# Performance work log

Hardware: AMD Instinct MI355X
Metric: run time of the kernel (lower is better)

Reference implementation:

```python
import jax, jax.numpy as jnp
import numpy as np

BETA = 0.25

def setup_inputs() -> dict:
    key = jax.random.key(0)
    k1, k2 = jax.random.split(key)
    x = jax.random.normal(k1, (16, 4096, 256), dtype=jnp.float32)
    emb = jax.random.normal(k2, (8, 1024, 256), dtype=jnp.float32)
    return {"x": x, "emb": emb}

def _quantize(r_flat, e):
    # r_flat: [N, D], e: [K, D]
    # squared-distance matrix: ||r||^2 + ||e||^2 - 2 r.e^T  -> [N, K]
    d = (jnp.sum(r_flat * r_flat, axis=1, keepdims=True)
         + jnp.sum(e * e, axis=1)
         - 2.0 * r_flat @ e.T)
    idx = jnp.argmin(d, axis=1)          # [N]
    z_q = jnp.take(e, idx, axis=0)       # [N, D] gather
    return z_q, idx

def reference(x, emb):
    # x: [B, T, D]; emb: [Q, K, D]
    B, T, D = x.shape
    Q = emb.shape[0]
    sg = jax.lax.stop_gradient
    residual = x
    quantized_out = jnp.zeros_like(x)
    total_loss = jnp.zeros((), dtype=x.dtype)
    indices = []
    for i in range(Q):  # sequential residual dependency (small fixed Q)
        r_flat = residual.reshape(-1, D)
        zq_flat, idx = _quantize(r_flat, emb[i])
        z_q = zq_flat.reshape(residual.shape)
        loss = (BETA * jnp.mean((sg(z_q) - residual) ** 2)
                + jnp.mean((z_q - sg(residual)) ** 2))
        z_q = residual + sg(z_q - residual)  # straight-through
        residual = residual - z_q
        quantized_out = quantized_out + z_q
        total_loss = total_loss + loss
        indices.append(idx.reshape(B, T))
    return quantized_out, total_loss, jnp.stack(indices, axis=-1)
```

## Files before the change

kernel.cpp:

```cpp
#include <hip/hip_runtime.h>


#define NROWS 65536
#define DDIM  256
#define KC    1024
#define QST   8
#define BR    64
#define MCAP  24

typedef __attribute__((ext_vector_type(8))) short short8;
typedef __attribute__((ext_vector_type(4))) float f32x4;
typedef unsigned int u32;
typedef unsigned short u16;

__device__ __forceinline__ u16 f2bf(float f) {
  u32 b = __float_as_uint(f);
  return (u16)((b + 0x7FFFu + ((b >> 16) & 1u)) >> 16);
}
__device__ __forceinline__ float bf2f(u16 h) {
  return __uint_as_float(((u32)h) << 16);
}
__device__ __forceinline__ u32 runit(int row, int u) {
  return (u32)(row * 1024 + ((u ^ (row & 7)) << 4));
}
__device__ __forceinline__ void gld16(const void* g, void* lds) {
  __builtin_amdgcn_global_load_lds((const __attribute__((address_space(1))) u32*)g,
                                   (__attribute__((address_space(3))) u32*)lds, 16, 0, 0);
}

__global__ void e2_kernel(const float* __restrict__ emb, float* __restrict__ e2) {
  const int row  = blockIdx.x * 4 + (threadIdx.x >> 6);
  const int lane = threadIdx.x & 63;
  const float4 v = ((const float4*)(emb + (size_t)row * DDIM))[lane];
  float s = v.x * v.x + v.y * v.y + v.z * v.z + v.w * v.w;
  #pragma unroll
  for (int m = 32; m >= 1; m >>= 1) s += __shfl_xor(s, m);
  if (lane == 0) e2[row] = s;
}

__global__ void pack_kernel(const float* __restrict__ emb, u16* __restrict__ packE) {
  const int t = blockIdx.x * 256 + threadIdx.x;
  const int l   = t & 63;
  const int ci  = (t >> 6) & 3;
  const int ekt = (t >> 8) & 7;
  const int ct  = (t >> 11) & 15;
  const int qi  = t >> 15;
  const int code = ct * 64 + ci * 16 + (l & 15);
  const int d0   = ekt * 32 + (l >> 4) * 8;
  const float* src = emb + ((size_t)qi * KC + code) * DDIM + d0;
  short8 v;
  #pragma unroll
  for (int j = 0; j < 8; ++j) v[j] = (short)f2bf(src[j]);
  *(short8*)(packE + (size_t)t * 8) = v;
}

__global__ __launch_bounds__(512, 2)
void rvq_kernel(const float* __restrict__ x, const float* __restrict__ emb,
                const char* __restrict__ packEb, const float* __restrict__ e2g,
                float* __restrict__ out, float* __restrict__ outIdx,
                float* __restrict__ lossPart)
{
  __shared__ __align__(16) u16  Rl[BR * 512];
  __shared__ __align__(16) char Bbuf[8][2][4096];
  __shared__ float e2L[KC];
  __shared__ float sredV[8][BR];
  __shared__ int   sredI[8][BR];
  __shared__ float d0L[BR];
  __shared__ int   cntL[BR];
  __shared__ int   candL[BR][MCAP];
  __shared__ int   sidx[BR];
  __shared__ float rnormL[BR];
  __shared__ float redbuf[8];

  const int tid = threadIdx.x;
  const int w = tid >> 6, l = tid & 63;
  const int g = l >> 4, rb16 = l & 15;
  const int row = tid >> 3, sub = tid & 7;
  const size_t rowBase = (size_t)blockIdx.x * BR;
  char* RlB = (char*)Rl;
  float lossAcc = 0.f;
  float r[32];

  {
    const float* xp = x + (rowBase + row) * DDIM + 32 * sub;
    float rn = 0.f;
    #pragma unroll
    for (int uu = 0; uu < 4; ++uu) {
      f32x4 va = *(const f32x4*)(xp + 8 * uu);
      f32x4 vb = *(const f32x4*)(xp + 8 * uu + 4);
      r[8*uu+0]=va.x; r[8*uu+1]=va.y; r[8*uu+2]=va.z; r[8*uu+3]=va.w;
      r[8*uu+4]=vb.x; r[8*uu+5]=vb.y; r[8*uu+6]=vb.z; r[8*uu+7]=vb.w;
      short8 hv, lv;
      #pragma unroll
      for (int j = 0; j < 8; ++j) {
        float v = r[8*uu+j];
        u16 h = f2bf(v); float hf = bf2f(h);
        hv[j] = (short)h; lv[j] = (short)f2bf(v - hf);
        rn += v * v;
      }
      *(short8*)(RlB + runit(row, 4*sub + uu))      = hv;
      *(short8*)(RlB + runit(row, 32 + 4*sub + uu)) = lv;
    }
    rn += __shfl_xor(rn, 1); rn += __shfl_xor(rn, 2); rn += __shfl_xor(rn, 4);
    if (sub == 0) rnormL[row] = rn;
  }
  __syncthreads();

  for (int qi = 0; qi < QST; ++qi) {
    e2L[tid]       = e2g[qi * KC + tid];
    e2L[tid + 512] = e2g[qi * KC + 512 + tid];
    __syncthreads();

    f32x4 acc[2][4][4];
    #pragma unroll
    for (int a = 0; a < 2; ++a)
      #pragma unroll
      for (int b = 0; b < 4; ++b)
        #pragma unroll
        for (int c2 = 0; c2 < 4; ++c2)
          acc[a][b][c2] = (f32x4){0.f, 0.f, 0.f, 0.f};

    const size_t stageBase = ((size_t)qi * 16 + 2 * w) * 8 * 4096;
    #define CHUNK_SRC(c) (packEb + stageBase + (size_t)(c) * 4096 + (size_t)l * 16)
    #define ISSUE(c) do { \
      const char* _g = CHUNK_SRC(c); \
      char* _d = &Bbuf[w][(c) & 1][0]; \
      gld16(_g,        _d);        gld16(_g + 1024, _d + 1024); \
      gld16(_g + 2048, _d + 2048); gld16(_g + 3072, _d + 3072); \
    } while (0)

    ISSUE(0);
    #pragma unroll
    for (int c = 0; c < 16; ++c) {
      if (c < 15) { ISSUE(c + 1); asm volatile("s_waitcnt vmcnt(4)" ::: "memory"); }
      else        {               asm volatile("s_waitcnt vmcnt(0)" ::: "memory"); }
      const char* bufc = &Bbuf[w][c & 1][0];
      const int ekt = c & 7, ctl = c >> 3;
      short8 Af[4];
      #pragma unroll
      for (int ci = 0; ci < 4; ++ci)
        Af[ci] = *(const short8*)(bufc + ci * 1024 + l * 16);
      #pragma unroll
      for (int ri = 0; ri < 4; ++ri) {
        short8 B = *(const short8*)(RlB + runit(16 * ri + rb16, ekt * 4 + g));
        #pragma unroll
        for (int ci = 0; ci < 4; ++ci)
          acc[ctl][ci][ri] = __builtin_amdgcn_mfma_f32_16x16x32_bf16(Af[ci], B, acc[ctl][ci][ri], 0, 0, 0);
      }
      #pragma unroll
      for (int ri = 0; ri < 4; ++ri) {
        short8 B = *(const short8*)(RlB + runit(16 * ri + rb16, 32 + ekt * 4 + g));
        #pragma unroll
        for (int ci = 0; ci < 4; ++ci)
          acc[ctl][ci][ri] = __builtin_amdgcn_mfma_f32_16x16x32_bf16(Af[ci], B, acc[ctl][ci][ri], 0, 0, 0);
      }
    }

    float bestV[4]; int bestI[4];
    #pragma unroll
    for (int ri = 0; ri < 4; ++ri) { bestV[ri] = 3.4e38f; bestI[ri] = 0; }
    #pragma unroll
    for (int ctl = 0; ctl < 2; ++ctl) {
      const int cb = (2 * w + ctl) * 64;
      #pragma unroll
      for (int ci = 0; ci < 4; ++ci) {
        f32x4 e4 = *(const f32x4*)&e2L[cb + 16 * ci + 4 * g];
        #pragma unroll
        for (int j = 0; j < 4; ++j) {
          const int code = cb + 16 * ci + 4 * g + j;
          #pragma unroll
          for (int ri = 0; ri < 4; ++ri) {
            float d = e4[j] - 2.f * acc[ctl][ci][ri][j];
            if (d < bestV[ri]) { bestV[ri] = d; bestI[ri] = code; }
          }
        }
      }
    }
    #pragma unroll
    for (int m = 16; m <= 32; m <<= 1) {
      #pragma unroll
      for (int ri = 0; ri < 4; ++ri) {
        float ov = __shfl_xor(bestV[ri], m);
        int   oi = __shfl_xor(bestI[ri], m);
        if (ov < bestV[ri] || (ov == bestV[ri] && oi < bestI[ri])) { bestV[ri] = ov; bestI[ri] = oi; }
      }
    }
    if (l < 16) {
      #pragma unroll
      for (int ri = 0; ri < 4; ++ri) { sredV[w][16*ri + l] = bestV[ri]; sredI[w][16*ri + l] = bestI[ri]; }
    }
    __syncthreads();

    if (tid < BR) {
      float dv = sredV[0][tid]; int di = sredI[0][tid];
      #pragma unroll
      for (int wv = 1; wv < 8; ++wv) {
        float v = sredV[wv][tid]; int ii = sredI[wv][tid];
        if (v < dv || (v == dv && ii < di)) { dv = v; di = ii; }
      }
      d0L[tid] = dv; sidx[tid] = di; cntL[tid] = 0;
    }
    __syncthreads();

    {
      float thr[4];
      #pragma unroll
      for (int ri = 0; ri < 4; ++ri) {
        const int rw = 16 * ri + rb16;
        thr[ri] = d0L[rw] + 0.36f * sqrtf(rnormL[rw]) + 0.05f;
      }
      #pragma unroll
      for (int ctl = 0; ctl < 2; ++ctl) {
        const int cb = (2 * w + ctl) * 64;
        #pragma unroll
        for (int ci = 0; ci < 4; ++ci) {
          f32x4 e4 = *(const f32x4*)&e2L[cb + 16 * ci + 4 * g];
          #pragma unroll
          for (int ri = 0; ri < 4; ++ri) {
            #pragma unroll
            for (int j = 0; j < 4; ++j) {
              float d = e4[j] - 2.f * acc[ctl][ci][ri][j];
              if (d <= thr[ri]) {
                const int rw = 16 * ri + rb16;
                int p = atomicAdd(&cntL[rw], 1);
                if (p < MCAP) candL[rw][p] = cb + 16 * ci + 4 * g + j;
              }
            }
          }
        }
      }
    }
    __syncthreads();

    {
      int cnt = cntL[row];
      if (cnt > 1) {
        if (cnt > MCAP) cnt = MCAP;
        float bd = 3.4e38f; int bi = 0x7fffffff;
        for (int k2 = 0; k2 < cnt; ++k2) {
          const int c = candL[row][k2];
          const float* ep = emb + ((size_t)qi * KC + c) * DDIM + 32 * sub;
          float dot = 0.f;
          #pragma unroll
          for (int f = 0; f < 8; ++f) {
            f32x4 ev = *(const f32x4*)(ep + 4 * f);
            dot += r[4*f+0]*ev.x + r[4*f+1]*ev.y + r[4*f+2]*ev.z + r[4*f+3]*ev.w;
          }
          dot += __shfl_xor(dot, 1); dot += __shfl_xor(dot, 2); dot += __shfl_xor(dot, 4);
          float d = e2L[c] - 2.f * dot;
          if (d < bd || (d == bd && c < bi)) { bd = d; bi = c; }
        }
        if (sub == 0) sidx[row] = bi;
      }
    }
    __syncthreads();

    {
      const int c = sidx[row];
      const float* ep = emb + ((size_t)qi * KC + c) * DDIM + 32 * sub;
      float ls = 0.f;
      #pragma unroll
      for (int f = 0; f < 8; ++f) {
        f32x4 ev = *(const f32x4*)(ep + 4 * f);
        r[4*f+0] -= ev.x; ls += r[4*f+0]*r[4*f+0];
        r[4*f+1] -= ev.y; ls += r[4*f+1]*r[4*f+1];
        r[4*f+2] -= ev.z; ls += r[4*f+2]*r[4*f+2];
        r[4*f+3] -= ev.w; ls += r[4*f+3]*r[4*f+3];
      }
      #pragma unroll
      for (int uu = 0; uu < 4; ++uu) {
        short8 hv, lv;
        #pragma unroll
        for (int j = 0; j < 8; ++j) {
          float v = r[8*uu+j];
          u16 h = f2bf(v); float hf = bf2f(h);
          hv[j] = (short)h; lv[j] = (short)f2bf(v - hf);
        }
        *(short8*)(RlB + runit(row, 4*sub + uu))      = hv;
        *(short8*)(RlB + runit(row, 32 + 4*sub + uu)) = lv;
      }
      float rn = ls;
      rn += __shfl_xor(rn, 1); rn += __shfl_xor(rn, 2); rn += __shfl_xor(rn, 4);
      if (sub == 0) rnormL[row] = rn;
      lossAcc += ls;
      if (tid < BR) outIdx[(rowBase + tid) * QST + qi] = (float)sidx[tid];
    }
    __syncthreads();
  }

  {
    const float* xp = x + (rowBase + row) * DDIM + 32 * sub;
    float* op = out + (rowBase + row) * DDIM + 32 * sub;
    #pragma unroll
    for (int f = 0; f < 8; ++f) {
      f32x4 xv = *(const f32x4*)(xp + 4 * f);
      f32x4 o;
      o.x = xv.x - r[4*f+0]; o.y = xv.y - r[4*f+1];
      o.z = xv.z - r[4*f+2]; o.w = xv.w - r[4*f+3];
      *(f32x4*)(op + 4 * f) = o;
    }
  }

  {
    float s = lossAcc;
    #pragma unroll
    for (int m = 32; m >= 1; m >>= 1) s += __shfl_xor(s, m);
    if (l == 0) redbuf[w] = s;
    __syncthreads();
    if (tid == 0) {
      float t2 = 0.f;
      #pragma unroll
      for (int wv = 0; wv < 8; ++wv) t2 += redbuf[wv];
      lossPart[blockIdx.x] = t2;
    }
  }
}

__global__ void loss_final(const float* __restrict__ part, float* __restrict__ outLoss) {
  __shared__ float buf[256];
  const int t = threadIdx.x;
  float s = 0.f;
  #pragma unroll
  for (int k = 0; k < 4; ++k) s += part[t + 256 * k];
  buf[t] = s;
  __syncthreads();
  for (int st = 128; st >= 1; st >>= 1) {
    if (t < st) buf[t] += buf[t + st];
    __syncthreads();
  }
  if (t == 0) *outLoss = buf[0] * (1.25f / 16777216.f);
}

extern "C" void kernel_launch(void* const* d_in, const int* in_sizes, int n_in,
                              void* d_out, int out_size, void* d_ws, size_t ws_size,
                              hipStream_t stream) {
  (void)in_sizes; (void)n_in; (void)out_size; (void)ws_size;
  const float* x   = (const float*)d_in[0];
  const float* emb = (const float*)d_in[1];
  float* out     = (float*)d_out;
  float* outLoss = out + (size_t)NROWS * DDIM;
  float* outIdx  = outLoss + 1;
  char*  packE   = (char*)d_ws;
  float* e2      = (float*)(packE + (size_t)QST*16*8*4*4096);
  float* part    = e2 + QST * KC;

  pack_kernel<<<dim3(1024), dim3(256), 0, stream>>>(emb, (u16*)packE);
  e2_kernel<<<dim3(QST * KC / 4), dim3(256), 0, stream>>>(emb, e2);
  rvq_kernel<<<dim3(NROWS / BR), dim3(512), 0, stream>>>(x, emb, packE, e2, out, outIdx, part);
  loss_final<<<dim3(1), dim3(256), 0, stream>>>(part, outLoss);
}
```

Before: 984.2 us.

## Drop bf16 hi/lo split residual and use 16 waves per block

The residual is now kept in LDS as a single bf16 copy instead of a hi+lo split pair, which halves the MFMA work in the distance GEMM. The block grows to 1024 threads (16 waves), each wave owning 64 codes with a 4-deep async LDS prefetch ring, and each row is handled by 16 threads. The lower-precision distances lean more on the existing candidate threshold refinement, and a new fallback scans all 1024 codes in fp32 when candidates overflow MCAP. That fallback keeps results exact but can be expensive if the threshold admits too many candidates.

```diff
diff --git a/kernel.cpp b/kernel.cpp
--- a/kernel.cpp
+++ b/kernel.cpp
@@ -17,11 +17,8 @@
   u32 b = __float_as_uint(f);
   return (u16)((b + 0x7FFFu + ((b >> 16) & 1u)) >> 16);
 }
-__device__ __forceinline__ float bf2f(u16 h) {
-  return __uint_as_float(((u32)h) << 16);
-}
 __device__ __forceinline__ u32 runit(int row, int u) {
-  return (u32)(row * 1024 + ((u ^ (row & 7)) << 4));
+  return (u32)(row * 512 + ((u ^ (row & 7)) << 4));
 }
 __device__ __forceinline__ void gld16(const void* g, void* lds) {
   __builtin_amdgcn_global_load_lds((const __attribute__((address_space(1))) u32*)g,
@@ -39,140 +36,112 @@
 }
 
 __global__ void pack_kernel(const float* __restrict__ emb, u16* __restrict__ packE) {
-  const int t = blockIdx.x * 256 + threadIdx.x;
-  const int l   = t & 63;
-  const int ci  = (t >> 6) & 3;
-  const int ekt = (t >> 8) & 7;
-  const int ct  = (t >> 11) & 15;
-  const int qi  = t >> 15;
-  const int code = ct * 64 + ci * 16 + (l & 15);
-  const int d0   = ekt * 32 + (l >> 4) * 8;
-  const float* src = emb + ((size_t)qi * KC + code) * DDIM + d0;
+  const int t  = blockIdx.x * 256 + threadIdx.x;
+  const int l  = t & 63;
+  const int c  = (t >> 6) & 31;
+  const int w  = (t >> 11) & 15;
+  const int qi = t >> 15;
+  const int code = 64 * w + 16 * (c & 3) + (l & 15);
+  const int k    = 32 * (c >> 2) + 8 * (l >> 4);
+  const float* src = emb + ((size_t)qi * KC + code) * DDIM + k;
   short8 v;
   #pragma unroll
   for (int j = 0; j < 8; ++j) v[j] = (short)f2bf(src[j]);
   *(short8*)(packE + (size_t)t * 8) = v;
 }
 
-__global__ __launch_bounds__(512, 2)
+__global__ __launch_bounds__(1024)
 void rvq_kernel(const float* __restrict__ x, const float* __restrict__ emb,
                 const char* __restrict__ packEb, const float* __restrict__ e2g,
                 float* __restrict__ out, float* __restrict__ outIdx,
                 float* __restrict__ lossPart)
 {
-  __shared__ __align__(16) u16  Rl[BR * 512];
-  __shared__ __align__(16) char Bbuf[8][2][4096];
+  __shared__ __align__(16) u16  Rh[BR * 256];
+  __shared__ __align__(16) char Bbuf[16][4][1024];
   __shared__ float e2L[KC];
-  __shared__ float sredV[8][BR];
-  __shared__ int   sredI[8][BR];
+  __shared__ float sredV[16][BR];
+  __shared__ int   sredI[16][BR];
   __shared__ float d0L[BR];
   __shared__ int   cntL[BR];
   __shared__ int   candL[BR][MCAP];
   __shared__ int   sidx[BR];
   __shared__ float rnormL[BR];
-  __shared__ float redbuf[8];
+  __shared__ float red[16];
 
   const int tid = threadIdx.x;
   const int w = tid >> 6, l = tid & 63;
-  const int g = l >> 4, rb16 = l & 15;
-  const int row = tid >> 3, sub = tid & 7;
+  const int row = tid >> 4, sub = tid & 15;
   const size_t rowBase = (size_t)blockIdx.x * BR;
-  char* RlB = (char*)Rl;
+  char* RhB = (char*)Rh;
   float lossAcc = 0.f;
-  float r[32];
+  float r[16];
 
   {
-    const float* xp = x + (rowBase + row) * DDIM + 32 * sub;
+    const float* xp = x + (rowBase + row) * DDIM + 16 * sub;
     float rn = 0.f;
     #pragma unroll
-    for (int uu = 0; uu < 4; ++uu) {
-      f32x4 va = *(const f32x4*)(xp + 8 * uu);
-      f32x4 vb = *(const f32x4*)(xp + 8 * uu + 4);
-      r[8*uu+0]=va.x; r[8*uu+1]=va.y; r[8*uu+2]=va.z; r[8*uu+3]=va.w;
-      r[8*uu+4]=vb.x; r[8*uu+5]=vb.y; r[8*uu+6]=vb.z; r[8*uu+7]=vb.w;
-      short8 hv, lv;
-      #pragma unroll
-      for (int j = 0; j < 8; ++j) {
-        float v = r[8*uu+j];
-        u16 h = f2bf(v); float hf = bf2f(h);
-        hv[j] = (short)h; lv[j] = (short)f2bf(v - hf);
-        rn += v * v;
-      }
-      *(short8*)(RlB + runit(row, 4*sub + uu))      = hv;
-      *(short8*)(RlB + runit(row, 32 + 4*sub + uu)) = lv;
-    }
-    rn += __shfl_xor(rn, 1); rn += __shfl_xor(rn, 2); rn += __shfl_xor(rn, 4);
+    for (int f = 0; f < 4; ++f) {
+      f32x4 v = *(const f32x4*)(xp + 4 * f);
+      r[4*f+0] = v.x; r[4*f+1] = v.y; r[4*f+2] = v.z; r[4*f+3] = v.w;
+      rn += v.x*v.x + v.y*v.y + v.z*v.z + v.w*v.w;
+    }
+    short8 h0, h1;
+    #pragma unroll
+    for (int j = 0; j < 8; ++j) { h0[j] = (short)f2bf(r[j]); h1[j] = (short)f2bf(r[8+j]); }
+    *(short8*)(RhB + runit(row, 2*sub))     = h0;
+    *(short8*)(RhB + runit(row, 2*sub + 1)) = h1;
+    rn += __shfl_xor(rn, 1); rn += __shfl_xor(rn, 2);
+    rn += __shfl_xor(rn, 4); rn += __shfl_xor(rn, 8);
     if (sub == 0) rnormL[row] = rn;
   }
   __syncthreads();
 
   for (int qi = 0; qi < QST; ++qi) {
-    e2L[tid]       = e2g[qi * KC + tid];
-    e2L[tid + 512] = e2g[qi * KC + 512 + tid];
-    __syncthreads();
-
-    f32x4 acc[2][4][4];
-    #pragma unroll
-    for (int a = 0; a < 2; ++a)
-      #pragma unroll
-      for (int b = 0; b < 4; ++b)
+    e2L[tid] = e2g[qi * KC + tid];
+
+    f32x4 acc[4][4];
+    #pragma unroll
+    for (int a = 0; a < 4; ++a)
+      #pragma unroll
+      for (int b = 0; b < 4; ++b) acc[a][b] = (f32x4){0.f, 0.f, 0.f, 0.f};
+
+    const char* src = packEb + ((size_t)(qi * 16 + w) * 32) * 1024 + (size_t)l * 16;
+    #define ISSUE(c) gld16(src + (size_t)(c) * 1024, &Bbuf[w][(c) & 3][0])
+    ISSUE(0); ISSUE(1); ISSUE(2);
+    for (int ekt = 0; ekt < 8; ++ekt) {
+      short8 Bf[4];
+      #pragma unroll
+      for (int ri = 0; ri < 4; ++ri)
+        Bf[ri] = *(const short8*)(RhB + runit(16 * ri + (l & 15), ekt * 4 + (l >> 4)));
+      #pragma unroll
+      for (int ci = 0; ci < 4; ++ci) {
+        const int c = ekt * 4 + ci;
+        if (c < 29)      { ISSUE(c + 3); asm volatile("s_waitcnt vmcnt(3)" ::: "memory"); }
+        else if (c == 29) asm volatile("s_waitcnt vmcnt(2)" ::: "memory");
+        else if (c == 30) asm volatile("s_waitcnt vmcnt(1)" ::: "memory");
+        else              asm volatile("s_waitcnt vmcnt(0)" ::: "memory");
+        const short8 Af = *(const short8*)(&Bbuf[w][c & 3][l * 16]);
         #pragma unroll
-        for (int c2 = 0; c2 < 4; ++c2)
-          acc[a][b][c2] = (f32x4){0.f, 0.f, 0.f, 0.f};
-
-    const size_t stageBase = ((size_t)qi * 16 + 2 * w) * 8 * 4096;
-    #define CHUNK_SRC(c) (packEb + stageBase + (size_t)(c) * 4096 + (size_t)l * 16)
-    #define ISSUE(c) do { \
-      const char* _g = CHUNK_SRC(c); \
-      char* _d = &Bbuf[w][(c) & 1][0]; \
-      gld16(_g,        _d);        gld16(_g + 1024, _d + 1024); \
-      gld16(_g + 2048, _d + 2048); gld16(_g + 3072, _d + 3072); \
-    } while (0)
-
-    ISSUE(0);
-    #pragma unroll
-    for (int c = 0; c < 16; ++c) {
-      if (c < 15) { ISSUE(c + 1); asm volatile("s_waitcnt vmcnt(4)" ::: "memory"); }
-      else        {               asm volatile("s_waitcnt vmcnt(0)" ::: "memory"); }
-      const char* bufc = &Bbuf[w][c & 1][0];
-      const int ekt = c & 7, ctl = c >> 3;
-      short8 Af[4];
-      #pragma unroll
-      for (int ci = 0; ci < 4; ++ci)
-        Af[ci] = *(const short8*)(bufc + ci * 1024 + l * 16);
-      #pragma unroll
-      for (int ri = 0; ri < 4; ++ri) {
-        short8 B = *(const short8*)(RlB + runit(16 * ri + rb16, ekt * 4 + g));
+        for (int ri = 0; ri < 4; ++ri)
+          acc[ci][ri] = __builtin_amdgcn_mfma_f32_16x16x32_bf16(Af, Bf[ri], acc[ci][ri], 0, 0, 0);
+      }
+    }
+    #undef ISSUE
+    __syncthreads();
+
+    float bestV[4]; int bestI[4];
+    #pragma unroll
+    for (int ri = 0; ri < 4; ++ri) { bestV[ri] = 3.4e38f; bestI[ri] = 0; }
+    #pragma unroll
+    for (int ci = 0; ci < 4; ++ci) {
+      const int cb = 64 * w + 16 * ci + 4 * (l >> 4);
+      f32x4 e4 = *(const f32x4*)&e2L[cb];
+      #pragma unroll
+      for (int jj = 0; jj < 4; ++jj) {
         #pragma unroll
-        for (int ci = 0; ci < 4; ++ci)
-          acc[ctl][ci][ri] = __builtin_amdgcn_mfma_f32_16x16x32_bf16(Af[ci], B, acc[ctl][ci][ri], 0, 0, 0);
-      }
-      #pragma unroll
-      for (int ri = 0; ri < 4; ++ri) {
-        short8 B = *(const short8*)(RlB + runit(16 * ri + rb16, 32 + ekt * 4 + g));
-        #pragma unroll
-        for (int ci = 0; ci < 4; ++ci)
-          acc[ctl][ci][ri] = __builtin_amdgcn_mfma_f32_16x16x32_bf16(Af[ci], B, acc[ctl][ci][ri], 0, 0, 0);
-      }
-    }
-
-    float bestV[4]; int bestI[4];
-    #pragma unroll
-    for (int ri = 0; ri < 4; ++ri) { bestV[ri] = 3.4e38f; bestI[ri] = 0; }
-    #pragma unroll
-    for (int ctl = 0; ctl < 2; ++ctl) {
-      const int cb = (2 * w + ctl) * 64;
-      #pragma unroll
-      for (int ci = 0; ci < 4; ++ci) {
-        f32x4 e4 = *(const f32x4*)&e2L[cb + 16 * ci + 4 * g];
-        #pragma unroll
-        for (int j = 0; j < 4; ++j) {
-          const int code = cb + 16 * ci + 4 * g + j;
-          #pragma unroll
-          for (int ri = 0; ri < 4; ++ri) {
-            float d = e4[j] - 2.f * acc[ctl][ci][ri][j];
-            if (d < bestV[ri]) { bestV[ri] = d; bestI[ri] = code; }
-          }
+        for (int ri = 0; ri < 4; ++ri) {
+          float d = e4[jj] - 2.f * acc[ci][ri][jj];
+          if (d < bestV[ri]) { bestV[ri] = d; bestI[ri] = cb + jj; }
         }
       }
     }
@@ -194,7 +163,7 @@
     if (tid < BR) {
       float dv = sredV[0][tid]; int di = sredI[0][tid];
       #pragma unroll
-      for (int wv = 1; wv < 8; ++wv) {
+      for (int wv = 1; wv < 16; ++wv) {
         float v = sredV[wv][tid]; int ii = sredI[wv][tid];
         if (v < dv || (v == dv && ii < di)) { dv = v; di = ii; }
       }
@@ -206,25 +175,22 @@
       float thr[4];
       #pragma unroll
       for (int ri = 0; ri < 4; ++ri) {
-        const int rw = 16 * ri + rb16;
+        const int rw = 16 * ri + (l & 15);
         thr[ri] = d0L[rw] + 0.36f * sqrtf(rnormL[rw]) + 0.05f;
       }
       #pragma unroll
-      for (int ctl = 0; ctl < 2; ++ctl) {
-        const int cb = (2 * w + ctl) * 64;
+      for (int ci = 0; ci < 4; ++ci) {
+        const int cb = 64 * w + 16 * ci + 4 * (l >> 4);
+        f32x4 e4 = *(const f32x4*)&e2L[cb];
         #pragma unroll
-        for (int ci = 0; ci < 4; ++ci) {
-          f32x4 e4 = *(const f32x4*)&e2L[cb + 16 * ci + 4 * g];
+        for (int jj = 0; jj < 4; ++jj) {
           #pragma unroll
           for (int ri = 0; ri < 4; ++ri) {
-            #pragma unroll
-            for (int j = 0; j < 4; ++j) {
-              float d = e4[j] - 2.f * acc[ctl][ci][ri][j];
-              if (d <= thr[ri]) {
-                const int rw = 16 * ri + rb16;
-                int p = atomicAdd(&cntL[rw], 1);
-                if (p < MCAP) candL[rw][p] = cb + 16 * ci + 4 * g + j;
-              }
+            float d = e4[jj] - 2.f * acc[ci][ri][jj];
+            if (d <= thr[ri]) {
+              const int rw = 16 * ri + (l & 15);
+              int p = atomicAdd(&cntL[rw], 1);
+              if (p < MCAP) candL[rw][p] = cb + jj;
             }
           }
         }
@@ -235,18 +201,19 @@
     {
       int cnt = cntL[row];
       if (cnt > 1) {
-        if (cnt > MCAP) cnt = MCAP;
         float bd = 3.4e38f; int bi = 0x7fffffff;
-        for (int k2 = 0; k2 < cnt; ++k2) {
-          const int c = candL[row][k2];
-          const float* ep = emb + ((size_t)qi * KC + c) * DDIM + 32 * sub;
+        const int n = (cnt <= MCAP) ? cnt : KC;
+        for (int k2 = 0; k2 < n; ++k2) {
+          const int c = (cnt <= MCAP) ? candL[row][k2] : k2;
+          const float* ep = emb + ((size_t)qi * KC + c) * DDIM + 16 * sub;
           float dot = 0.f;
           #pragma unroll
-          for (int f = 0; f < 8; ++f) {
+          for (int f = 0; f < 4; ++f) {
             f32x4 ev = *(const f32x4*)(ep + 4 * f);
             dot += r[4*f+0]*ev.x + r[4*f+1]*ev.y + r[4*f+2]*ev.z + r[4*f+3]*ev.w;
           }
-          dot += __shfl_xor(dot, 1); dot += __shfl_xor(dot, 2); dot += __shfl_xor(dot, 4);
+          dot += __shfl_xor(dot, 1); dot += __shfl_xor(dot, 2);
+          dot += __shfl_xor(dot, 4); dot += __shfl_xor(dot, 8);
           float d = e2L[c] - 2.f * dot;
           if (d < bd || (d == bd && c < bi)) { bd = d; bi = c; }
         }
@@ -257,42 +224,36 @@
 
     {
       const int c = sidx[row];
-      const float* ep = emb + ((size_t)qi * KC + c) * DDIM + 32 * sub;
+      const float* ep = emb + ((size_t)qi * KC + c) * DDIM + 16 * sub;
       float ls = 0.f;
       #pragma unroll
-      for (int f = 0; f < 8; ++f) {
+      for (int f = 0; f < 4; ++f) {
         f32x4 ev = *(const f32x4*)(ep + 4 * f);
         r[4*f+0] -= ev.x; ls += r[4*f+0]*r[4*f+0];
         r[4*f+1] -= ev.y; ls += r[4*f+1]*r[4*f+1];
         r[4*f+2] -= ev.z; ls += r[4*f+2]*r[4*f+2];
         r[4*f+3] -= ev.w; ls += r[4*f+3]*r[4*f+3];
       }
-      #pragma unroll
-      for (int uu = 0; uu < 4; ++uu) {
-        short8 hv, lv;
-        #pragma unroll
-        for (int j = 0; j < 8; ++j) {
-          float v = r[8*uu+j];
-          u16 h = f2bf(v); float hf = bf2f(h);
-          hv[j] = (short)h; lv[j] = (short)f2bf(v - hf);
-        }
-        *(short8*)(RlB + runit(row, 4*sub + uu))      = hv;
-        *(short8*)(RlB + runit(row, 32 + 4*sub + uu)) = lv;
-      }
+      short8 h0, h1;
+      #pragma unroll
+      for (int j = 0; j < 8; ++j) { h0[j] = (short)f2bf(r[j]); h1[j] = (short)f2bf(r[8+j]); }
+      *(short8*)(RhB + runit(row, 2*sub))     = h0;
+      *(short8*)(RhB + runit(row, 2*sub + 1)) = h1;
+      lossAcc += ls;
       float rn = ls;
-      rn += __shfl_xor(rn, 1); rn += __shfl_xor(rn, 2); rn += __shfl_xor(rn, 4);
+      rn += __shfl_xor(rn, 1); rn += __shfl_xor(rn, 2);
+      rn += __shfl_xor(rn, 4); rn += __shfl_xor(rn, 8);
       if (sub == 0) rnormL[row] = rn;
-      lossAcc += ls;
       if (tid < BR) outIdx[(rowBase + tid) * QST + qi] = (float)sidx[tid];
     }
     __syncthreads();
   }
 
   {
-    const float* xp = x + (rowBase + row) * DDIM + 32 * sub;
-    float* op = out + (rowBase + row) * DDIM + 32 * sub;
-    #pragma unroll
-    for (int f = 0; f < 8; ++f) {
+    const float* xp = x + (rowBase + row) * DDIM + 16 * sub;
+    float* op = out + (rowBase + row) * DDIM + 16 * sub;
+    #pragma unroll
+    for (int f = 0; f < 4; ++f) {
       f32x4 xv = *(const f32x4*)(xp + 4 * f);
       f32x4 o;
       o.x = xv.x - r[4*f+0]; o.y = xv.y - r[4*f+1];
@@ -305,12 +266,12 @@
     float s = lossAcc;
     #pragma unroll
     for (int m = 32; m >= 1; m >>= 1) s += __shfl_xor(s, m);
-    if (l == 0) redbuf[w] = s;
+    if (l == 0) red[w] = s;
     __syncthreads();
     if (tid == 0) {
       float t2 = 0.f;
       #pragma unroll
-      for (int wv = 0; wv < 8; ++wv) t2 += redbuf[wv];
+      for (int wv = 0; wv < 16; ++wv) t2 += red[wv];
       lossPart[blockIdx.x] = t2;
     }
   }
@@ -341,11 +302,11 @@
   float* outLoss = out + (size_t)NROWS * DDIM;
   float* outIdx  = outLoss + 1;
   char*  packE   = (char*)d_ws;
-  float* e2      = (float*)(packE + (size_t)QST*16*8*4*4096);
+  float* e2      = (float*)(packE + (size_t)QST * 16 * 32 * 1024);
   float* part    = e2 + QST * KC;
 
   pack_kernel<<<dim3(1024), dim3(256), 0, stream>>>(emb, (u16*)packE);
   e2_kernel<<<dim3(QST * KC / 4), dim3(256), 0, stream>>>(emb, e2);
-  rvq_kernel<<<dim3(NROWS / BR), dim3(512), 0, stream>>>(x, emb, packE, e2, out, outIdx, part);
+  rvq_kernel<<<dim3(NROWS / BR), dim3(1024), 0, stream>>>(x, emb, packE, e2, out, outIdx, part);
   loss_final<<<dim3(1), dim3(256), 0, stream>>>(part, outLoss);
 }
```

Measured after the change: 877.2 us. -10.9%, faster.
